# Performance work log

Measured on AMD Instinct MI355X. Metric: run time of the kernel, lower is better.

The kernel has to match this reference:

```python
import jax, jax.numpy as jnp
import numpy as np
import math

B, S, D, H, F, L = 16, 512, 1024, 16, 4096, 4
DK = D // H
NEG = -1e32


def _cosine_pe(max_len, d_model):
    # deterministic sin/cos table (the 0.1*randn init is fully overwritten for even d_model)
    pos = np.arange(max_len, dtype=np.float32)[:, None]
    div = np.exp(np.arange(0, d_model, 2, dtype=np.float32) * (-(math.log(10000.0) / d_model)))
    pe = np.zeros((max_len, d_model), dtype=np.float32)
    pe[:, 0::2] = np.sin(pos * div)
    pe[:, 1::2] = np.cos(pos * div)
    return jnp.asarray(pe)[None]  # [1, max_len, D]


def setup_inputs() -> dict:
    key = jax.random.key(0)
    ks = jax.random.split(key, 16)
    sc_d = 1.0 / math.sqrt(D)
    sc_f = 1.0 / math.sqrt(F)
    return {
        "q_embed_data": jax.random.normal(ks[0], (B, S, D), jnp.float32),
        "qa_embed_data": jax.random.normal(ks[1], (B, S, D), jnp.float32),
        "pe": _cosine_pe(S, D),
        "Wk": jax.random.normal(ks[2], (L, D, D), jnp.float32) * sc_d,
        "bk": jnp.zeros((L, D), jnp.float32),
        "Wv": jax.random.normal(ks[3], (L, D, D), jnp.float32) * sc_d,
        "bv": jnp.zeros((L, D), jnp.float32),
        "Wo": jax.random.normal(ks[4], (L, D, D), jnp.float32) * sc_d,
        "bo": jnp.zeros((L, D), jnp.float32),
        "ln1_g": jnp.ones((L, D), jnp.float32),
        "ln1_b": jnp.zeros((L, D), jnp.float32),
        "W1": jax.random.normal(ks[5], (L, D, F), jnp.float32) * sc_d,
        "b1": jnp.zeros((L, F), jnp.float32),
        "W2": jax.random.normal(ks[6], (L, F, D), jnp.float32) * sc_f,
        "b2": jnp.zeros((L, D), jnp.float32),
        "ln2_g": jnp.ones((L, D), jnp.float32),
        "ln2_b": jnp.zeros((L, D), jnp.float32),
    }


def _layer_norm(x, g, b, eps=1e-5):
    mu = jnp.mean(x, axis=-1, keepdims=True)
    var = jnp.var(x, axis=-1, keepdims=True)
    return (x - mu) * jax.lax.rsqrt(var + eps) * g + b


def _forward(q_embed_data, qa_embed_data, pe, Wk, bk, Wv, bv, Wo, bo,
             ln1_g, ln1_b, W1, b1, W2, b2, ln2_g, ln2_b):
    x = q_embed_data + pe[:, :S, :]
    y = qa_embed_data + pe[:, :S, :]  # values stay fixed across blocks
    # mask=0 in TransformerLayer: triu(k=0)==0 -> strictly-lower-triangular allowed
    allowed = jnp.tril(jnp.ones((S, S), bool), k=-1)  # [S, S]
    row_keep = (jnp.arange(S) > 0).astype(x.dtype)[None, None, :, None]  # zero_pad row 0
    scale = 1.0 / math.sqrt(DK)
    for l in range(L):
        # kq_same: q and k both use k_linear
        qk = (x @ Wk[l] + bk[l]).reshape(B, S, H, DK).transpose(0, 2, 1, 3)  # [B,H,S,DK]
        v = (y @ Wv[l] + bv[l]).reshape(B, S, H, DK).transpose(0, 2, 1, 3)
        scores = jnp.einsum('bhqd,bhkd->bhqk', qk, qk) * scale
        scores = jnp.where(allowed, scores, NEG)
        attn = jax.nn.softmax(scores, axis=-1) * row_keep  # zero_pad: first query row -> zeros
        ctx = jnp.einsum('bhqk,bhkd->bhqd', attn, v)
        ctx = ctx.transpose(0, 2, 1, 3).reshape(B, S, D)
        x = _layer_norm(x + (ctx @ Wo[l] + bo[l]), ln1_g[l], ln1_b[l])
        ffn = jax.nn.relu(x @ W1[l] + b1[l]) @ W2[l] + b2[l]
        x = _layer_norm(x + ffn, ln2_g[l], ln2_b[l])
    return x


def reference(q_embed_data, qa_embed_data, pe, Wk, bk, Wv, bv, Wo, bo,
              ln1_g, ln1_b, W1, b1, W2, b2, ln2_g, ln2_b):
    return _forward(q_embed_data, qa_embed_data, pe, Wk, bk, Wv, bv, Wo, bo,
                    ln1_g, ln1_b, W1, b1, W2, b2, ln2_g, ln2_b)
```

## Files before the change

kernel.cpp:

```cpp
#include <hip/hip_runtime.h>
#include <stdint.h>

typedef unsigned short u16;
typedef __bf16 bf16x8 __attribute__((ext_vector_type(8)));
typedef float f32x4 __attribute__((ext_vector_type(4)));

#define BDIM 16
#define SLEN 512
#define DMODEL 1024
#define NHEAD 16
#define DHEAD 64
#define FDIM 4096
#define NLAYER 4
#define ROWS (BDIM*SLEN)
#define KVT 64
#define QBLK 128

__device__ __forceinline__ u16 f2b(float f) {
  uint32_t u = __builtin_bit_cast(uint32_t, f);
  u = (u + 0x7fffu + ((u >> 16) & 1u)) >> 16;
  return (u16)u;
}
__device__ __forceinline__ float b2f(u16 u) {
  return __builtin_bit_cast(float, (uint32_t)u << 16);
}
__device__ __forceinline__ float b2f_lo(uint32_t u) {
  return __builtin_bit_cast(float, u << 16);
}
__device__ __forceinline__ float b2f_hi(uint32_t u) {
  return __builtin_bit_cast(float, u & 0xffff0000u);
}

__device__ __forceinline__ void gl_lds16(const void* g, void* l) {
  uint32_t loff = (uint32_t)(uintptr_t)l;
  __builtin_amdgcn_global_load_lds(
      (__attribute__((address_space(1))) uint32_t*)(uintptr_t)g,
      (__attribute__((address_space(3))) uint32_t*)loff,
      16, 0, 0);
}

__global__ __launch_bounds__(256) void prep_kernel(const float4* __restrict__ q,
                                                   const float4* __restrict__ qa,
                                                   const float4* __restrict__ pe,
                                                   u16* __restrict__ xb,
                                                   u16* __restrict__ yb) {
  int idx = blockIdx.x * 256 + threadIdx.x;
  int pidx = idx & (SLEN * DMODEL / 4 - 1);
  float4 qv = q[idx], av = qa[idx], pv = pe[pidx];
  uint32_t x0 = (uint32_t)f2b(qv.x + pv.x) | ((uint32_t)f2b(qv.y + pv.y) << 16);
  uint32_t x1 = (uint32_t)f2b(qv.z + pv.z) | ((uint32_t)f2b(qv.w + pv.w) << 16);
  uint32_t y0 = (uint32_t)f2b(av.x + pv.x) | ((uint32_t)f2b(av.y + pv.y) << 16);
  uint32_t y1 = (uint32_t)f2b(av.z + pv.z) | ((uint32_t)f2b(av.w + pv.w) << 16);
  ((uint2*)xb)[idx] = make_uint2(x0, x1);
  ((uint2*)yb)[idx] = make_uint2(y0, y1);
}

__global__ __launch_bounds__(256) void transpose_f2b(const float* __restrict__ in,
                                                     u16* __restrict__ out,
                                                     int M, int N) {
  __shared__ float t[32][33];
  int tx = threadIdx.x & 31, ty = threadIdx.x >> 5;
  int m0 = blockIdx.y * 32, n0 = blockIdx.x * 32;
  const float* inz = in + (size_t)blockIdx.z * M * N;
  u16* outz = out + (size_t)blockIdx.z * M * N;
  #pragma unroll
  for (int i = 0; i < 32; i += 8) t[ty + i][tx] = inz[(size_t)(m0 + ty + i) * N + n0 + tx];
  __syncthreads();
  #pragma unroll
  for (int i = 0; i < 32; i += 8) outz[(size_t)(n0 + ty + i) * M + m0 + tx] = f2b(t[tx][ty + i]);
}

template<int BN, bool RELU, bool BF16OUT>
__global__ __launch_bounds__(512, 2) void gemm8p(const u16* __restrict__ Ap,
                                                 const u16* __restrict__ Bp,
                                                 const float* __restrict__ bias,
                                                 void* __restrict__ Cp,
                                                 int M, int N, int K) {
  constexpr int NBH = BN / 128;
  constexpr int NREP = BN / 64;
  constexpr int QN = NREP / 2;
  constexpr int HU = 8192;
  __shared__ __attribute__((aligned(16))) u16 lds[2][(2 + NBH) * HU];

  const int tid = threadIdx.x, wave = tid >> 6, lane = tid & 63;
  const int lg = lane >> 4, lc = lane & 15;
  const int wm = wave >> 2, wn = wave & 3;

  const int gx = gridDim.x;
  int nwg = gx * gridDim.y;
  int orig = blockIdx.y * gx + blockIdx.x;
  int qq = nwg >> 3, rr_ = nwg & 7;
  int xcd = orig & 7, ix = orig >> 3;
  int wg = (xcd < rr_ ? xcd * (qq + 1) : rr_ * (qq + 1) + (xcd - rr_) * qq) + ix;
  const int m0 = (wg / gx) * 256, n0 = (wg % gx) * BN;

  const int ldbyte = K * 2;
  const char* Ag = (const char*)Ap + (size_t)m0 * ldbyte;
  const char* Bg = (const char*)Bp + (size_t)n0 * ldbyte;

  int o1 = tid * 16, o2 = 8192 + tid * 16;
  int sr1 = o1 >> 7, sg1 = (((o1 >> 4) & 7) - sr1) & 7;
  int sr2 = o2 >> 7, sg2 = (((o2 >> 4) & 7) - sr2) & 7;
  const int soff1 = sr1 * ldbyte + sg1 * 16;
  const int soff2 = sr2 * ldbyte + sg2 * 16;
  const int NT = K >> 6;

  auto stageA = [&](int kt, int h, int buf) {
    const char* g = Ag + (size_t)h * 128 * ldbyte + (size_t)kt * 128;
    char* d = (char*)&lds[buf][h * HU] + wave * 1024;
    gl_lds16(g + soff1, d);
    gl_lds16(g + soff2, d + 8192);
  };
  auto stageB = [&](int kt, int h, int buf) {
    const char* g = Bg + (size_t)h * 128 * ldbyte + (size_t)kt * 128;
    char* d = (char*)&lds[buf][(2 + h) * HU] + wave * 1024;
    gl_lds16(g + soff1, d);
    gl_lds16(g + soff2, d + 8192);
  };

  const int bstart = wn * (BN / 4);
  const int bh = bstart >> 7, bc0 = bstart & 127;

  auto rdA = [&](const u16* base, int f, int kk) -> bf16x8 {
    int row = f * 16 + lc;
    return *(const bf16x8*)&base[row * 64 + (((kk * 4 + lg + row) & 7) << 3)];
  };
  auto rdB = [&](const u16* base, int jj, int kk) -> bf16x8 {
    int row = bc0 + jj * 16 + lc;
    return *(const bf16x8*)&base[row * 64 + (((kk * 4 + lg + row) & 7) << 3)];
  };

  f32x4 acc[8][NREP];
  #pragma unroll
  for (int f = 0; f < 8; f++)
    #pragma unroll
    for (int j = 0; j < NREP; j++) acc[f][j] = (f32x4){0.f, 0.f, 0.f, 0.f};

  stageA(0, 0, 0); stageA(0, 1, 0);
  stageB(0, 0, 0); if (NBH == 2) stageB(0, 1, 0);
  stageA(1, 0, 1); stageA(1, 1, 1);
  asm volatile("s_waitcnt vmcnt(4)\n\ts_barrier" ::: "memory");

  auto ktile = [&](int k, int buf) {
    const u16* Ab_ = &lds[buf][wm * HU];
    const u16* Bb_ = &lds[buf][(2 + bh) * HU];
    const int kn = (k + 1 < NT) ? k + 1 : NT - 1;
    const int k2 = (k + 2 < NT) ? k + 2 : NT - 1;
    bf16x8 a0[4][2], a1[4][2], b0[QN][2], b1[QN][2];

    #pragma unroll
    for (int f = 0; f < 4; f++) { a0[f][0] = rdA(Ab_, f, 0); a0[f][1] = rdA(Ab_, f, 1); }
    #pragma unroll
    for (int j = 0; j < QN; j++) { b0[j][0] = rdB(Bb_, j, 0); b0[j][1] = rdB(Bb_, j, 1); }
    stageB(kn, 0, buf ^ 1);
    asm volatile("s_barrier" ::: "memory");
    __builtin_amdgcn_s_setprio(1);
    #pragma unroll
    for (int f = 0; f < 4; f++)
      #pragma unroll
      for (int j = 0; j < QN; j++) {
        acc[f][j] = __builtin_amdgcn_mfma_f32_16x16x32_bf16(a0[f][0], b0[j][0], acc[f][j], 0, 0, 0);
        acc[f][j] = __builtin_amdgcn_mfma_f32_16x16x32_bf16(a0[f][1], b0[j][1], acc[f][j], 0, 0, 0);
      }
    __builtin_amdgcn_s_setprio(0);
    asm volatile("s_barrier" ::: "memory");

    #pragma unroll
    for (int f = 0; f < 4; f++) { a1[f][0] = rdA(Ab_, 4 + f, 0); a1[f][1] = rdA(Ab_, 4 + f, 1); }
    if (NBH == 2) stageB(kn, 1, buf ^ 1);
    asm volatile("s_barrier" ::: "memory");
    __builtin_amdgcn_s_setprio(1);
    #pragma unroll
    for (int f = 0; f < 4; f++)
      #pragma unroll
      for (int j = 0; j < QN; j++) {
        acc[4 + f][j] = __builtin_amdgcn_mfma_f32_16x16x32_bf16(a1[f][0], b0[j][0], acc[4 + f][j], 0, 0, 0);
        acc[4 + f][j] = __builtin_amdgcn_mfma_f32_16x16x32_bf16(a1[f][1], b0[j][1], acc[4 + f][j], 0, 0, 0);
      }
    __builtin_amdgcn_s_setprio(0);
    asm volatile("s_barrier" ::: "memory");

    #pragma unroll
    for (int j = 0; j < QN; j++) { b1[j][0] = rdB(Bb_, QN + j, 0); b1[j][1] = rdB(Bb_, QN + j, 1); }
    stageA(k2, 0, buf);
    asm volatile("s_barrier" ::: "memory");
    __builtin_amdgcn_s_setprio(1);
    #pragma unroll
    for (int f = 0; f < 4; f++)
      #pragma unroll
      for (int j = 0; j < QN; j++) {
        acc[4 + f][QN + j] = __builtin_amdgcn_mfma_f32_16x16x32_bf16(a1[f][0], b1[j][0], acc[4 + f][QN + j], 0, 0, 0);
        acc[4 + f][QN + j] = __builtin_amdgcn_mfma_f32_16x16x32_bf16(a1[f][1], b1[j][1], acc[4 + f][QN + j], 0, 0, 0);
      }
    __builtin_amdgcn_s_setprio(0);
    asm volatile("s_barrier" ::: "memory");

    stageA(k2, 1, buf);
    asm volatile("s_barrier" ::: "memory");
    __builtin_amdgcn_s_setprio(1);
    #pragma unroll
    for (int f = 0; f < 4; f++)
      #pragma unroll
      for (int j = 0; j < QN; j++) {
        acc[f][QN + j] = __builtin_amdgcn_mfma_f32_16x16x32_bf16(a0[f][0], b1[j][0], acc[f][QN + j], 0, 0, 0);
        acc[f][QN + j] = __builtin_amdgcn_mfma_f32_16x16x32_bf16(a0[f][1], b1[j][1], acc[f][QN + j], 0, 0, 0);
      }
    __builtin_amdgcn_s_setprio(0);
    asm volatile("s_waitcnt vmcnt(4)\n\ts_barrier" ::: "memory");
  };

  for (int k = 0; k < NT; k += 2) {
    ktile(k, 0);
    ktile(k + 1, 1);
  }

  #pragma unroll
  for (int f = 0; f < 8; f++) {
    int row = m0 + wm * 128 + f * 16 + lg * 4;
    #pragma unroll
    for (int j = 0; j < NREP; j++) {
      int col = n0 + bstart + j * 16 + lc;
      float bv = bias[col];
      #pragma unroll
      for (int t2 = 0; t2 < 4; t2++) {
        float v = acc[f][j][t2] + bv;
        if (RELU) v = fmaxf(v, 0.f);
        if (BF16OUT) ((u16*)Cp)[(size_t)(row + t2) * N + col] = f2b(v);
        else         ((float*)Cp)[(size_t)(row + t2) * N + col] = v;
      }
    }
  }
}

template<bool RESID>
__global__ __launch_bounds__(256, 2) void gemm4w(const u16* __restrict__ Ap,
                                                 const u16* __restrict__ Bp,
                                                 const float* __restrict__ bias,
                                                 const u16* __restrict__ Rp,
                                                 u16* __restrict__ Cp,
                                                 int M, int N, int K) {
  __shared__ __attribute__((aligned(16))) u16 As[2][128 * 64];
  __shared__ __attribute__((aligned(16))) u16 Bs[2][128 * 64];
  const int tid = threadIdx.x, wave = tid >> 6, lane = tid & 63;
  const int lg = lane >> 4, lc = lane & 15;
  const int wm = wave >> 1, wn = wave & 1;

  const int gx = gridDim.x;
  int nwg = gx * gridDim.y;
  int orig = blockIdx.y * gx + blockIdx.x;
  int qq = nwg >> 3, rr_ = nwg & 7;
  int xcd = orig & 7, ix = orig >> 3;
  int wg = (xcd < rr_ ? xcd * (qq + 1) : rr_ * (qq + 1) + (xcd - rr_) * qq) + ix;
  const int m0 = (wg / gx) * 128, n0 = (wg % gx) * 128;

  const int ldbyte = K * 2;
  const char* Ag = (const char*)Ap + (size_t)m0 * ldbyte;
  const char* Bg = (const char*)Bp + (size_t)n0 * ldbyte;
  const int NT = K >> 6;

  auto stage = [&](const char* gb, int kt, u16* lb) {
    #pragma unroll
    for (int c = 0; c < 4; c++) {
      int o = c * 4096 + tid * 16;
      int row = o >> 7;
      int g = (((o >> 4) & 7) - row) & 7;
      gl_lds16(gb + (size_t)row * ldbyte + (size_t)kt * 128 + g * 16,
               (char*)lb + c * 4096 + wave * 1024);
    }
  };
  auto rd = [&](const u16* base, int strip, int f, int kk) -> bf16x8 {
    int row = strip * 64 + f * 16 + lc;
    return *(const bf16x8*)&base[row * 64 + (((kk * 4 + lg + row) & 7) << 3)];
  };

  f32x4 acc[4][4];
  #pragma unroll
  for (int f = 0; f < 4; f++)
    #pragma unroll
    for (int n = 0; n < 4; n++) acc[f][n] = (f32x4){0.f, 0.f, 0.f, 0.f};

  stage(Ag, 0, As[0]); stage(Bg, 0, Bs[0]);
  stage(Ag, 1, As[1]); stage(Bg, 1, Bs[1]);
  asm volatile("s_waitcnt vmcnt(8)\n\ts_barrier" ::: "memory");

  for (int k = 0; k < NT; k++) {
    const int buf = k & 1;
    const int k2 = (k + 2 < NT) ? k + 2 : k;
    bf16x8 a[4][2], b[4][2];
    #pragma unroll
    for (int f = 0; f < 4; f++) { a[f][0] = rd(As[buf], wm, f, 0); a[f][1] = rd(As[buf], wm, f, 1); }
    #pragma unroll
    for (int n = 0; n < 4; n++) { b[n][0] = rd(Bs[buf], wn, n, 0); b[n][1] = rd(Bs[buf], wn, n, 1); }
    asm volatile("s_barrier" ::: "memory");
    __builtin_amdgcn_s_setprio(1);
    #pragma unroll
    for (int f = 0; f < 4; f++)
      #pragma unroll
      for (int n = 0; n < 2; n++) {
        acc[f][n] = __builtin_amdgcn_mfma_f32_16x16x32_bf16(a[f][0], b[n][0], acc[f][n], 0, 0, 0);
        acc[f][n] = __builtin_amdgcn_mfma_f32_16x16x32_bf16(a[f][1], b[n][1], acc[f][n], 0, 0, 0);
      }
    __builtin_amdgcn_s_setprio(0);
    asm volatile("s_waitcnt lgkmcnt(0)\n\ts_barrier" ::: "memory");
    stage(Ag, k2, As[buf]);
    stage(Bg, k2, Bs[buf]);
    __builtin_amdgcn_s_setprio(1);
    #pragma unroll
    for (int f = 0; f < 4; f++)
      #pragma unroll
      for (int n = 2; n < 4; n++) {
        acc[f][n] = __builtin_amdgcn_mfma_f32_16x16x32_bf16(a[f][0], b[n][0], acc[f][n], 0, 0, 0);
        acc[f][n] = __builtin_amdgcn_mfma_f32_16x16x32_bf16(a[f][1], b[n][1], acc[f][n], 0, 0, 0);
      }
    __builtin_amdgcn_s_setprio(0);
    asm volatile("s_waitcnt vmcnt(8)\n\ts_barrier" ::: "memory");
  }

  #pragma unroll
  for (int f = 0; f < 4; f++) {
    int row = m0 + wm * 64 + f * 16 + lg * 4;
    #pragma unroll
    for (int n = 0; n < 4; n++) {
      int col = n0 + wn * 64 + n * 16 + lc;
      float bv = bias[col];
      #pragma unroll
      for (int r = 0; r < 4; r++) {
        float v = acc[f][n][r] + bv;
        if (RESID) v += b2f(Rp[(size_t)(row + r) * N + col]);
        Cp[(size_t)(row + r) * N + col] = f2b(v);
      }
    }
  }
}

__global__ __launch_bounds__(256, 2) void attn_kernel(const u16* __restrict__ QK,
                                                      const u16* __restrict__ V,
                                                      u16* __restrict__ CTX) {
  __shared__ __attribute__((aligned(16))) u16 Ks[2][KVT * 64];
  __shared__ __attribute__((aligned(16))) u16 VTs[64 * 72];
  __shared__ __attribute__((aligned(16))) u16 Ps[4][32 * 72];
  const int qt = blockIdx.x, bh = blockIdx.y;
  const int b = bh >> 4, h = bh & 15;
  const char* Qg = (const char*)(QK + (size_t)b * SLEN * DMODEL + h * DHEAD);
  const char* Vg = (const char*)(V + (size_t)b * SLEN * DMODEL + h * DHEAD);
  const int tid = threadIdx.x, wave = tid >> 6, lane = tid & 63;
  const int lg = lane >> 4, lc = lane & 15;
  const int ktmax = (qt * QBLK + QBLK - 2) >> 6;

  auto stageK = [&](int kt, int buf) {
    #pragma unroll
    for (int i = 0; i < 2; i++) {
      int o = i * 4096 + tid * 16;
      int row = o >> 7, slot = (o >> 4) & 7;
      int g = (slot - row) & 7;
      gl_lds16(Qg + (size_t)(kt * KVT + row) * (DMODEL * 2) + g * 16,
               (char*)Ks[buf] + i * 4096 + wave * 1024);
    }
  };
  const int vhi = lane >> 5, vls = lane & 31;
  const int vc_ = wave + 4 * vhi;
  auto loadV = [&](int kt, uint4 (&va)[2]) {
    const char* src = Vg + (size_t)(kt * KVT + 2 * vls) * (DMODEL * 2) + vc_ * 16;
    va[0] = *(const uint4*)src;
    va[1] = *(const uint4*)(src + DMODEL * 2);
  };
  auto writeVT = [&](const uint4 (&va)[2]) {
    u16 e0[8], e1[8];
    *(uint4*)e0 = va[0];
    *(uint4*)e1 = va[1];
    #pragma unroll
    for (int j = 0; j < 8; j++) {
      uint32_t pk = (uint32_t)e0[j] | ((uint32_t)e1[j] << 16);
      *(uint32_t*)&VTs[(8 * vc_ + j) * 72 + 2 * vls] = pk;
    }
  };

  uint4 vaA[2], vaB[2];
  bf16x8 aq[2][2];
  #pragma unroll
  for (int f = 0; f < 2; f++) {
    const int qrow = qt * QBLK + wave * 32 + f * 16 + lc;
    aq[f][0] = *(const bf16x8*)(Qg + (size_t)qrow * (DMODEL * 2) + lg * 16);
    aq[f][1] = *(const bf16x8*)(Qg + (size_t)qrow * (DMODEL * 2) + 64 + lg * 16);
  }
  stageK(0, 0);
  loadV(0, vaA);
  stageK(1, 1);
  asm volatile("s_waitcnt vmcnt(2)\n\ts_barrier" ::: "memory");

  float l_run[2][4] = {{0.f, 0.f, 0.f, 0.f}, {0.f, 0.f, 0.f, 0.f}};
  f32x4 acc_o[2][4];
  #pragma unroll
  for (int f = 0; f < 2; f++)
    #pragma unroll
    for (int n = 0; n < 4; n++) acc_o[f][n] = (f32x4){0.f, 0.f, 0.f, 0.f};

  auto iter = [&](int kt, int cur, uint4 (&vc)[2], uint4 (&vn)[2]) {
    const int kn = (kt + 1 <= ktmax) ? kt + 1 : ktmax;
    const int k2 = (kt + 2 <= ktmax) ? kt + 2 : kt;

    asm volatile("s_waitcnt vmcnt(2) lgkmcnt(0)" ::: "memory");
    __builtin_amdgcn_s_barrier();
    writeVT(vc);
    loadV(kn, vn);

    f32x4 sc[2][4];
    #pragma unroll
    for (int f = 0; f < 2; f++)
      #pragma unroll
      for (int n = 0; n < 4; n++) sc[f][n] = (f32x4){0.f, 0.f, 0.f, 0.f};
    #pragma unroll
    for (int n = 0; n < 4; n++) {
      int row = n * 16 + lc;
      bf16x8 bk0 = *(const bf16x8*)&Ks[cur][row * 64 + (((lg + row) & 7) << 3)];
      bf16x8 bk1 = *(const bf16x8*)&Ks[cur][row * 64 + (((4 + lg + row) & 7) << 3)];
      #pragma unroll
      for (int f = 0; f < 2; f++) {
        sc[f][n] = __builtin_amdgcn_mfma_f32_16x16x32_bf16(aq[f][0], bk0, sc[f][n], 0, 0, 0);
        sc[f][n] = __builtin_amdgcn_mfma_f32_16x16x32_bf16(aq[f][1], bk1, sc[f][n], 0, 0, 0);
      }
    }

    #pragma unroll
    for (int f = 0; f < 2; f++) {
      const int qbase = qt * QBLK + wave * 32 + f * 16 + lg * 4;
      #pragma unroll
      for (int n = 0; n < 4; n++) {
        int kg = kt * KVT + n * 16 + lc;
        #pragma unroll
        for (int r = 0; r < 4; r++) {
          float e = __expf(fmaf(sc[f][n][r], 0.125f, -24.f));
          float p = (kg < qbase + r) ? e : 0.f;
          l_run[f][r] += p;
          Ps[wave][(f * 16 + lg * 4 + r) * 72 + n * 16 + lc] = f2b(p);
        }
      }
    }

    asm volatile("s_waitcnt lgkmcnt(0)" ::: "memory");
    __builtin_amdgcn_s_barrier();
    stageK(k2, cur);

    bf16x8 ap[2][2];
    #pragma unroll
    for (int f = 0; f < 2; f++) {
      ap[f][0] = *(const bf16x8*)&Ps[wave][(f * 16 + lc) * 72 + lg * 8];
      ap[f][1] = *(const bf16x8*)&Ps[wave][(f * 16 + lc) * 72 + 32 + lg * 8];
    }
    #pragma unroll
    for (int n2 = 0; n2 < 4; n2++) {
      bf16x8 bv0 = *(const bf16x8*)&VTs[(n2 * 16 + lc) * 72 + lg * 8];
      bf16x8 bv1 = *(const bf16x8*)&VTs[(n2 * 16 + lc) * 72 + 32 + lg * 8];
      #pragma unroll
      for (int f = 0; f < 2; f++) {
        acc_o[f][n2] = __builtin_amdgcn_mfma_f32_16x16x32_bf16(ap[f][0], bv0, acc_o[f][n2], 0, 0, 0);
        acc_o[f][n2] = __builtin_amdgcn_mfma_f32_16x16x32_bf16(ap[f][1], bv1, acc_o[f][n2], 0, 0, 0);
      }
    }
  };

  for (int kt = 0; kt <= ktmax; kt += 2) {
    iter(kt, 0, vaA, vaB);
    iter(kt + 1, 1, vaB, vaA);
  }

  #pragma unroll
  for (int d = 1; d < 16; d <<= 1)
    #pragma unroll
    for (int f = 0; f < 2; f++)
      #pragma unroll
      for (int r = 0; r < 4; r++) l_run[f][r] += __shfl_xor(l_run[f][r], d, 64);

  asm volatile("s_waitcnt vmcnt(0)" ::: "memory");
  #pragma unroll
  for (int f = 0; f < 2; f++)
    #pragma unroll
    for (int n2 = 0; n2 < 4; n2++)
      #pragma unroll
      for (int r = 0; r < 4; r++) {
        int sq = qt * QBLK + wave * 32 + f * 16 + lg * 4 + r;
        float v = (sq == 0) ? 0.f : acc_o[f][n2][r] / l_run[f][r];
        CTX[((size_t)b * SLEN + sq) * DMODEL + h * DHEAD + n2 * 16 + lc] = f2b(v);
      }
}

template<bool OUT32>
__global__ __launch_bounds__(256) void ln_kernel(const u16* __restrict__ tmp,
                                                 u16* __restrict__ xb,
                                                 const float* __restrict__ gw,
                                                 const float* __restrict__ bw,
                                                 float4* __restrict__ outf) {
  __shared__ float red[4], red2[4];
  const int row = blockIdx.x, t = threadIdx.x;
  const size_t base = (size_t)row * DMODEL + t * 4;
  uint2 tv = *(const uint2*)&tmp[base];
  float v[4];
  v[0] = b2f_lo(tv.x); v[1] = b2f_hi(tv.x);
  v[2] = b2f_lo(tv.y); v[3] = b2f_hi(tv.y);
  float s = v[0] + v[1] + v[2] + v[3];
  #pragma unroll
  for (int d = 1; d < 64; d <<= 1) s += __shfl_xor(s, d, 64);
  if ((t & 63) == 0) red[t >> 6] = s;
  __syncthreads();
  float mean = (red[0] + red[1] + red[2] + red[3]) * (1.f / DMODEL);
  float q2 = 0.f;
  #pragma unroll
  for (int i = 0; i < 4; i++) { float d_ = v[i] - mean; q2 += d_ * d_; }
  #pragma unroll
  for (int d = 1; d < 64; d <<= 1) q2 += __shfl_xor(q2, d, 64);
  if ((t & 63) == 0) red2[t >> 6] = q2;
  __syncthreads();
  float var = (red2[0] + red2[1] + red2[2] + red2[3]) * (1.f / DMODEL);
  float rs = rsqrtf(var + 1e-5f);
  float4 gv = *(const float4*)&gw[t * 4];
  float4 bv4 = *(const float4*)&bw[t * 4];
  float o0 = (v[0] - mean) * rs * gv.x + bv4.x;
  float o1 = (v[1] - mean) * rs * gv.y + bv4.y;
  float o2 = (v[2] - mean) * rs * gv.z + bv4.z;
  float o3 = (v[3] - mean) * rs * gv.w + bv4.w;
  if (OUT32) {
    outf[(size_t)row * (DMODEL / 4) + t] =
        make_float4(b2f(f2b(o0)), b2f(f2b(o1)), b2f(f2b(o2)), b2f(f2b(o3)));
  } else {
    uint2 pk;
    pk.x = (uint32_t)f2b(o0) | ((uint32_t)f2b(o1) << 16);
    pk.y = (uint32_t)f2b(o2) | ((uint32_t)f2b(o3) << 16);
    *(uint2*)&xb[base] = pk;
  }
}

extern "C" void kernel_launch(void* const* d_in, const int* in_sizes, int n_in,
                              void* d_out, int out_size, void* d_ws, size_t ws_size,
                              hipStream_t stream) {
  (void)in_sizes; (void)n_in; (void)out_size;
  const float* q    = (const float*)d_in[0];
  const float* qa   = (const float*)d_in[1];
  const float* pe   = (const float*)d_in[2];
  const float* Wk   = (const float*)d_in[3];
  const float* bk   = (const float*)d_in[4];
  const float* Wv   = (const float*)d_in[5];
  const float* bv   = (const float*)d_in[6];
  const float* Wo   = (const float*)d_in[7];
  const float* bo   = (const float*)d_in[8];
  const float* ln1g = (const float*)d_in[9];
  const float* ln1b = (const float*)d_in[10];
  const float* W1   = (const float*)d_in[11];
  const float* b1   = (const float*)d_in[12];
  const float* W2   = (const float*)d_in[13];
  const float* b2   = (const float*)d_in[14];
  const float* ln2g = (const float*)d_in[15];
  const float* ln2b = (const float*)d_in[16];

  char* w = (char*)d_ws;
  u16* xb   = (u16*)w; w += (size_t)ROWS * DMODEL * 2;
  u16* yb   = (u16*)w; w += (size_t)ROWS * DMODEL * 2;
  u16* qkb  = (u16*)w; w += (size_t)ROWS * DMODEL * 2;
  u16* vb   = (u16*)w; w += (size_t)ROWS * DMODEL * 2;
  u16* ctxb = (u16*)w; w += (size_t)ROWS * DMODEL * 2;
  u16* ffnb = (u16*)w; w += (size_t)ROWS * FDIM * 2;
  u16* tmpb = qkb;

  const size_t DD = (size_t)DMODEL * DMODEL, DF = (size_t)DMODEL * FDIM;
  size_t used = (size_t)(w - (char*)d_ws);
  const bool hoist = ws_size >= used + (3 * DD + 2 * DF) * NLAYER * 2;

  u16 *WkT, *WvT, *WoT, *W1T, *W2T;
  if (hoist) {
    WkT = (u16*)w; w += DD * NLAYER * 2;
    WvT = (u16*)w; w += DD * NLAYER * 2;
    WoT = (u16*)w; w += DD * NLAYER * 2;
    W1T = (u16*)w; w += DF * NLAYER * 2;
    W2T = (u16*)w; w += DF * NLAYER * 2;
  } else {
    WkT = (u16*)w; w += DD * 2;
    WvT = (u16*)w; w += DD * 2;
    WoT = (u16*)w; w += DD * 2;
    W1T = (u16*)w; w += DF * 2;
    W2T = (u16*)w; w += DF * 2;
  }

  prep_kernel<<<ROWS * DMODEL / 4 / 256, 256, 0, stream>>>(
      (const float4*)q, (const float4*)qa, (const float4*)pe, xb, yb);

  if (hoist) {
    transpose_f2b<<<dim3(32, 32, NLAYER), 256, 0, stream>>>(Wk, WkT, DMODEL, DMODEL);
    transpose_f2b<<<dim3(32, 32, NLAYER), 256, 0, stream>>>(Wv, WvT, DMODEL, DMODEL);
    transpose_f2b<<<dim3(32, 32, NLAYER), 256, 0, stream>>>(Wo, WoT, DMODEL, DMODEL);
    transpose_f2b<<<dim3(128, 32, NLAYER), 256, 0, stream>>>(W1, W1T, DMODEL, FDIM);
    transpose_f2b<<<dim3(32, 128, NLAYER), 256, 0, stream>>>(W2, W2T, FDIM, DMODEL);
  }

  for (int l = 0; l < NLAYER; l++) {
    u16 *WkTl, *WvTl, *WoTl, *W1Tl, *W2Tl;
    if (hoist) {
      WkTl = WkT + l * DD; WvTl = WvT + l * DD; WoTl = WoT + l * DD;
      W1Tl = W1T + l * DF; W2Tl = W2T + l * DF;
    } else {
      transpose_f2b<<<dim3(32, 32), 256, 0, stream>>>(Wk + l * DD, WkT, DMODEL, DMODEL);
      transpose_f2b<<<dim3(32, 32), 256, 0, stream>>>(Wv + l * DD, WvT, DMODEL, DMODEL);
      transpose_f2b<<<dim3(32, 32), 256, 0, stream>>>(Wo + l * DD, WoT, DMODEL, DMODEL);
      transpose_f2b<<<dim3(128, 32), 256, 0, stream>>>(W1 + l * DF, W1T, DMODEL, FDIM);
      transpose_f2b<<<dim3(32, 128), 256, 0, stream>>>(W2 + l * DF, W2T, FDIM, DMODEL);
      WkTl = WkT; WvTl = WvT; WoTl = WoT; W1Tl = W1T; W2Tl = W2T;
    }

    gemm4w<false><<<dim3(DMODEL / 128, ROWS / 128), 256, 0, stream>>>(
        xb, WkTl, bk + l * DMODEL, nullptr, qkb, ROWS, DMODEL, DMODEL);
    gemm4w<false><<<dim3(DMODEL / 128, ROWS / 128), 256, 0, stream>>>(
        yb, WvTl, bv + l * DMODEL, nullptr, vb, ROWS, DMODEL, DMODEL);
    attn_kernel<<<dim3(SLEN / QBLK, BDIM * NHEAD), 256, 0, stream>>>(qkb, vb, ctxb);
    gemm4w<true><<<dim3(DMODEL / 128, ROWS / 128), 256, 0, stream>>>(
        ctxb, WoTl, bo + l * DMODEL, xb, tmpb, ROWS, DMODEL, DMODEL);
    ln_kernel<false><<<ROWS, 256, 0, stream>>>(tmpb, xb, ln1g + l * DMODEL, ln1b + l * DMODEL, nullptr);
    gemm8p<256, true, true><<<dim3(FDIM / 256, ROWS / 256), 512, 0, stream>>>(
        xb, W1Tl, b1 + l * FDIM, ffnb, ROWS, FDIM, DMODEL);
    gemm4w<true><<<dim3(DMODEL / 128, ROWS / 128), 256, 0, stream>>>(
        ffnb, W2Tl, b2 + l * DMODEL, xb, tmpb, ROWS, DMODEL, FDIM);
    if (l == NLAYER - 1) {
      ln_kernel<true><<<ROWS, 256, 0, stream>>>(tmpb, xb, ln2g + l * DMODEL, ln2b + l * DMODEL,
                                                (float4*)d_out);
    } else {
      ln_kernel<false><<<ROWS, 256, 0, stream>>>(tmpb, xb, ln2g + l * DMODEL, ln2b + l * DMODEL, nullptr);
    }
  }
}
```

Before: 1.133 ms.

## Halve gemm4w K-tile to raise occupancy and merge K/V projections into one launch

The 128x128 GEMM kernel now stages 32-wide K slices instead of 64, halving LDS use and register fragments so launch bounds can allow four blocks per CU instead of two. The swizzle pattern is adapted to the narrower tile. The K and V projection GEMMs are fused into a single launch using a z-dimension of two, doubling the grid for that stage. Each K step now has half as many MFMAs between barriers, so synchronisation and staging overhead per FLOP roughly doubles in exchange for more resident waves.

```diff
diff --git a/kernel.cpp b/kernel.cpp
--- a/kernel.cpp
+++ b/kernel.cpp
@@ -232,18 +232,24 @@
   }
 }
 
-template<bool RESID>
-__global__ __launch_bounds__(256, 2) void gemm4w(const u16* __restrict__ Ap,
+template<bool RESID, bool DUAL>
+__global__ __launch_bounds__(256, 4) void gemm4w(const u16* __restrict__ Ap,
                                                  const u16* __restrict__ Bp,
                                                  const float* __restrict__ bias,
                                                  const u16* __restrict__ Rp,
                                                  u16* __restrict__ Cp,
+                                                 const u16* __restrict__ Ap2,
+                                                 const u16* __restrict__ Bp2,
+                                                 const float* __restrict__ bias2,
+                                                 u16* __restrict__ Cp2,
                                                  int M, int N, int K) {
-  __shared__ __attribute__((aligned(16))) u16 As[2][128 * 64];
-  __shared__ __attribute__((aligned(16))) u16 Bs[2][128 * 64];
+  __shared__ __attribute__((aligned(16))) u16 As[2][128 * 32];
+  __shared__ __attribute__((aligned(16))) u16 Bs[2][128 * 32];
   const int tid = threadIdx.x, wave = tid >> 6, lane = tid & 63;
   const int lg = lane >> 4, lc = lane & 15;
   const int wm = wave >> 1, wn = wave & 1;
+
+  if (DUAL && blockIdx.z == 1) { Ap = Ap2; Bp = Bp2; bias = bias2; Cp = Cp2; }
 
   const int gx = gridDim.x;
   int nwg = gx * gridDim.y;
@@ -256,21 +262,22 @@
   const int ldbyte = K * 2;
   const char* Ag = (const char*)Ap + (size_t)m0 * ldbyte;
   const char* Bg = (const char*)Bp + (size_t)n0 * ldbyte;
-  const int NT = K >> 6;
+  const int NT = K >> 5;
 
   auto stage = [&](const char* gb, int kt, u16* lb) {
     #pragma unroll
-    for (int c = 0; c < 4; c++) {
+    for (int c = 0; c < 2; c++) {
       int o = c * 4096 + tid * 16;
-      int row = o >> 7;
-      int g = (((o >> 4) & 7) - row) & 7;
-      gl_lds16(gb + (size_t)row * ldbyte + (size_t)kt * 128 + g * 16,
+      int row = o >> 6;
+      int slot = (o >> 4) & 3;
+      int g = (slot - (row >> 1)) & 3;
+      gl_lds16(gb + (size_t)row * ldbyte + (size_t)kt * 64 + g * 16,
                (char*)lb + c * 4096 + wave * 1024);
     }
   };
-  auto rd = [&](const u16* base, int strip, int f, int kk) -> bf16x8 {
+  auto rd = [&](const u16* base, int strip, int f) -> bf16x8 {
     int row = strip * 64 + f * 16 + lc;
-    return *(const bf16x8*)&base[row * 64 + (((kk * 4 + lg + row) & 7) << 3)];
+    return *(const bf16x8*)&base[row * 32 + (((lg + (row >> 1)) & 3) << 3)];
   };
 
   f32x4 acc[4][4];
@@ -281,25 +288,23 @@
 
   stage(Ag, 0, As[0]); stage(Bg, 0, Bs[0]);
   stage(Ag, 1, As[1]); stage(Bg, 1, Bs[1]);
-  asm volatile("s_waitcnt vmcnt(8)\n\ts_barrier" ::: "memory");
+  asm volatile("s_waitcnt vmcnt(4)\n\ts_barrier" ::: "memory");
 
   for (int k = 0; k < NT; k++) {
     const int buf = k & 1;
     const int k2 = (k + 2 < NT) ? k + 2 : k;
-    bf16x8 a[4][2], b[4][2];
-    #pragma unroll
-    for (int f = 0; f < 4; f++) { a[f][0] = rd(As[buf], wm, f, 0); a[f][1] = rd(As[buf], wm, f, 1); }
-    #pragma unroll
-    for (int n = 0; n < 4; n++) { b[n][0] = rd(Bs[buf], wn, n, 0); b[n][1] = rd(Bs[buf], wn, n, 1); }
+    bf16x8 a[4], b[4];
+    #pragma unroll
+    for (int f = 0; f < 4; f++) a[f] = rd(As[buf], wm, f);
+    #pragma unroll
+    for (int n = 0; n < 4; n++) b[n] = rd(Bs[buf], wn, n);
     asm volatile("s_barrier" ::: "memory");
     __builtin_amdgcn_s_setprio(1);
     #pragma unroll
     for (int f = 0; f < 4; f++)
       #pragma unroll
-      for (int n = 0; n < 2; n++) {
-        acc[f][n] = __builtin_amdgcn_mfma_f32_16x16x32_bf16(a[f][0], b[n][0], acc[f][n], 0, 0, 0);
-        acc[f][n] = __builtin_amdgcn_mfma_f32_16x16x32_bf16(a[f][1], b[n][1], acc[f][n], 0, 0, 0);
-      }
+      for (int n = 0; n < 2; n++)
+        acc[f][n] = __builtin_amdgcn_mfma_f32_16x16x32_bf16(a[f], b[n], acc[f][n], 0, 0, 0);
     __builtin_amdgcn_s_setprio(0);
     asm volatile("s_waitcnt lgkmcnt(0)\n\ts_barrier" ::: "memory");
     stage(Ag, k2, As[buf]);
@@ -308,12 +313,10 @@
     #pragma unroll
     for (int f = 0; f < 4; f++)
       #pragma unroll
-      for (int n = 2; n < 4; n++) {
-        acc[f][n] = __builtin_amdgcn_mfma_f32_16x16x32_bf16(a[f][0], b[n][0], acc[f][n], 0, 0, 0);
-        acc[f][n] = __builtin_amdgcn_mfma_f32_16x16x32_bf16(a[f][1], b[n][1], acc[f][n], 0, 0, 0);
-      }
+      for (int n = 2; n < 4; n++)
+        acc[f][n] = __builtin_amdgcn_mfma_f32_16x16x32_bf16(a[f], b[n], acc[f][n], 0, 0, 0);
     __builtin_amdgcn_s_setprio(0);
-    asm volatile("s_waitcnt vmcnt(8)\n\ts_barrier" ::: "memory");
+    asm volatile("s_waitcnt vmcnt(4)\n\ts_barrier" ::: "memory");
   }
 
   #pragma unroll
@@ -604,18 +607,19 @@
       WkTl = WkT; WvTl = WvT; WoTl = WoT; W1Tl = W1T; W2Tl = W2T;
     }
 
-    gemm4w<false><<<dim3(DMODEL / 128, ROWS / 128), 256, 0, stream>>>(
-        xb, WkTl, bk + l * DMODEL, nullptr, qkb, ROWS, DMODEL, DMODEL);
-    gemm4w<false><<<dim3(DMODEL / 128, ROWS / 128), 256, 0, stream>>>(
-        yb, WvTl, bv + l * DMODEL, nullptr, vb, ROWS, DMODEL, DMODEL);
+    gemm4w<false, true><<<dim3(DMODEL / 128, ROWS / 128, 2), 256, 0, stream>>>(
+        xb, WkTl, bk + l * DMODEL, nullptr, qkb,
+        yb, WvTl, bv + l * DMODEL, vb, ROWS, DMODEL, DMODEL);
     attn_kernel<<<dim3(SLEN / QBLK, BDIM * NHEAD), 256, 0, stream>>>(qkb, vb, ctxb);
-    gemm4w<true><<<dim3(DMODEL / 128, ROWS / 128), 256, 0, stream>>>(
-        ctxb, WoTl, bo + l * DMODEL, xb, tmpb, ROWS, DMODEL, DMODEL);
+    gemm4w<true, false><<<dim3(DMODEL / 128, ROWS / 128), 256, 0, stream>>>(
+        ctxb, WoTl, bo + l * DMODEL, xb, tmpb,
+        nullptr, nullptr, nullptr, nullptr, ROWS, DMODEL, DMODEL);
     ln_kernel<false><<<ROWS, 256, 0, stream>>>(tmpb, xb, ln1g + l * DMODEL, ln1b + l * DMODEL, nullptr);
     gemm8p<256, true, true><<<dim3(FDIM / 256, ROWS / 256), 512, 0, stream>>>(
         xb, W1Tl, b1 + l * FDIM, ffnb, ROWS, FDIM, DMODEL);
-    gemm4w<true><<<dim3(DMODEL / 128, ROWS / 128), 256, 0, stream>>>(
-        ffnb, W2Tl, b2 + l * DMODEL, xb, tmpb, ROWS, DMODEL, FDIM);
+    gemm4w<true, false><<<dim3(DMODEL / 128, ROWS / 128), 256, 0, stream>>>(
+        ffnb, W2Tl, b2 + l * DMODEL, xb, tmpb,
+        nullptr, nullptr, nullptr, nullptr, ROWS, DMODEL, FDIM);
     if (l == NLAYER - 1) {
       ln_kernel<true><<<ROWS, 256, 0, stream>>>(tmpb, xb, ln2g + l * DMODEL, ln2b + l * DMODEL,
                                                 (float4*)d_out);
```

Result: slower. 1.201 ms (+6.1%).
